# Kernel tuning notes

Measured on AMD Instinct MI355X. Metric: run time of the kernel, lower is better.

Reference implementation:

```python
import jax, jax.numpy as jnp
import numpy as np

INIT_STDEV = 0.01

def setup_inputs() -> dict:
    key = jax.random.key(0)
    k1, k2, k3 = jax.random.split(key, 3)
    B, S, D = 8, 4096, 768
    x = jax.random.normal(k1, (B, S, D), dtype=jnp.float32)
    att_v = jax.random.normal(k2, (D,), dtype=jnp.float32) * INIT_STDEV
    att_W = jax.random.normal(k3, (D, D), dtype=jnp.float32) * INIT_STDEV
    return {"x": x, "att_v": att_v, "att_W": att_W}

def reference(x, att_v, att_W):
    # y = x @ W : [B,S,D]; scores = tanh(y) . v over D : [B,S]
    y = jnp.tanh(jnp.einsum('bsd,de->bse', x, att_W))
    scores = jnp.einsum('bsd,d->bs', y, att_v)
    weights = jax.nn.softmax(scores, axis=-1)            # softmax over sequence
    out = jnp.einsum('bs,bsd->bd', weights, x)           # attsum pool
    return out.astype(jnp.float32)
```

## Files before the change

kernel.cpp:

```cpp
#include <hip/hip_runtime.h>
#include <hip/hip_bf16.h>

constexpr int Bb = 8;
constexpr int Ss = 4096;
constexpr int Dd = 768;
constexpr int Mm = Bb * Ss;

typedef __bf16 bf16x8 __attribute__((ext_vector_type(8)));
typedef float f32x4 __attribute__((ext_vector_type(4)));

__device__ __forceinline__ float fast_tanh(float x) {
    return 1.f - 2.f / (__expf(2.f * x) + 1.f);
}

__device__ __forceinline__ void load_lds16(const void* g, void* l) {
    __builtin_amdgcn_global_load_lds(
        (const __attribute__((address_space(1))) unsigned int*)g,
        (__attribute__((address_space(3))) unsigned int*)l, 16, 0, 0);
}

__global__ __launch_bounds__(256) void convW(const float* __restrict__ W,
                                             __bf16* __restrict__ Wt) {
    __shared__ float tile[32][33];
    const int tx = threadIdx.x & 31;
    const int ty = threadIdx.x >> 5;
    const int kb = blockIdx.x * 32;
    const int nb = blockIdx.y * 32;
#pragma unroll
    for (int i = 0; i < 32; i += 8)
        tile[ty + i][tx] = W[(size_t)(kb + ty + i) * Dd + nb + tx];
    __syncthreads();
#pragma unroll
    for (int i = 0; i < 32; i += 8) {
        const int n = nb + ty + i;
        const int txs = (tx & 7) | ((((tx >> 3) & 3) ^ ((n >> 1) & 3)) << 3);
        Wt[(size_t)n * Dd + kb + txs] = (__bf16)tile[tx][ty + i];
    }
}

__global__ __launch_bounds__(512, 4) void scores_gemm(
    const float* __restrict__ x, const __bf16* __restrict__ Wt,
    const float* __restrict__ v, float* __restrict__ scores3) {
    __shared__ float  As[2][4096];
    __shared__ __bf16 Bs[3][256 * 32];

    const int t = threadIdx.x;
    const int id = blockIdx.x;
    const int ids = ((id & 7) * 96) + (id >> 3);
    const int mb = ids / 3;
    const int nb = ids - mb * 3;
    const int lane = t & 63;
    const int wave = t >> 6;
    const int wm = wave >> 2;
    const int wn = wave & 3;
    const int quad = lane >> 4;
    const int lid = lane & 15;
    const int rslot = ((quad ^ ((lid >> 1) & 3)) * 8);

    const int sarow = t >> 2;
    const float* axg0 = x + (size_t)(mb * 128 + sarow) * Dd + (t & 3) * 4;
    const float* axg1 = x + (size_t)(mb * 128 + sarow) * Dd + 16 + (((t & 3) ^ 1) * 4);

    const __bf16* bgp[2];
    int blp[2];
#pragma unroll
    for (int j = 0; j < 2; ++j) {
        const int flat = j * 8192 + t * 16;
        const int col = flat >> 6;
        bgp[j] = Wt + (size_t)(nb * 256 + col) * Dd + ((flat & 63) >> 1);
        blp[j] = flat >> 1;
    }

    const int p_ = quad >> 1;
    const int sA0 = ((quad & 1) * 2 + 0) ^ p_;
    const int sA1 = ((quad & 1) * 2 + 1) ^ p_;
    const int abase = p_ * 2048 + sA0 * 4;
    const int abase1 = p_ * 2048 + sA1 * 4;

    f32x4 acc[4][4];
#pragma unroll
    for (int tm = 0; tm < 4; ++tm)
#pragma unroll
        for (int nt = 0; nt < 4; ++nt) acc[tm][nt] = (f32x4){0.f, 0.f, 0.f, 0.f};

    load_lds16(axg0, &As[0][t * 4]);
    load_lds16(axg1, &As[0][2048 + t * 4]);
#pragma unroll
    for (int j = 0; j < 2; ++j) load_lds16(bgp[j], &Bs[0][blp[j]]);
#pragma unroll
    for (int j = 0; j < 2; ++j) load_lds16(bgp[j] + 32, &Bs[1][blp[j]]);

#pragma unroll
    for (int k = 0; k < 24; ++k) {
        if (k == 23) asm volatile("s_waitcnt vmcnt(0)" ::: "memory");
        else         asm volatile("s_waitcnt vmcnt(2)" ::: "memory");
        __builtin_amdgcn_sched_barrier(0);
        __builtin_amdgcn_s_barrier();
        __builtin_amdgcn_sched_barrier(0);

        if (k < 23) {
            load_lds16(axg0 + (k + 1) * 32, &As[(k + 1) & 1][t * 4]);
            load_lds16(axg1 + (k + 1) * 32, &As[(k + 1) & 1][2048 + t * 4]);
        }
        if (k < 22) {
#pragma unroll
            for (int j = 0; j < 2; ++j)
                load_lds16(bgp[j] + (k + 2) * 32, &Bs[(k + 2) % 3][blp[j]]);
        }
        __builtin_amdgcn_sched_barrier(0);

        bf16x8 af[4], bfr[4];
#pragma unroll
        for (int tm = 0; tm < 4; ++tm) {
            const int row = wm * 64 + tm * 16 + lid;
            const f32x4 r1 = *(const f32x4*)(&As[k & 1][abase + row * 16]);
            const f32x4 r2 = *(const f32x4*)(&As[k & 1][abase1 + row * 16]);
            bf16x8 a;
            a[0] = (__bf16)r1[0]; a[1] = (__bf16)r1[1];
            a[2] = (__bf16)r1[2]; a[3] = (__bf16)r1[3];
            a[4] = (__bf16)r2[0]; a[5] = (__bf16)r2[1];
            a[6] = (__bf16)r2[2]; a[7] = (__bf16)r2[3];
            af[tm] = a;
        }
#pragma unroll
        for (int nt = 0; nt < 4; ++nt)
            bfr[nt] = *(const bf16x8*)(&Bs[k % 3][(wn * 64 + nt * 16 + lid) * 32 + rslot]);

        __builtin_amdgcn_s_setprio(1);
#pragma unroll
        for (int tm = 0; tm < 4; ++tm)
#pragma unroll
            for (int nt = 0; nt < 4; ++nt)
                acc[tm][nt] = __builtin_amdgcn_mfma_f32_16x16x32_bf16(af[tm], bfr[nt], acc[tm][nt], 0, 0, 0);
        __builtin_amdgcn_s_setprio(0);
    }

    __syncthreads();
    float* ssc = (float*)&Bs[0][0];

    float vv[4];
#pragma unroll
    for (int nt = 0; nt < 4; ++nt)
        vv[nt] = v[nb * 256 + wn * 64 + nt * 16 + lid];

#pragma unroll
    for (int tm = 0; tm < 4; ++tm)
#pragma unroll
        for (int r = 0; r < 4; ++r) {
            float s = 0.f;
#pragma unroll
            for (int nt = 0; nt < 4; ++nt) s += vv[nt] * fast_tanh(acc[tm][nt][r]);
            s += __shfl_xor(s, 1);
            s += __shfl_xor(s, 2);
            s += __shfl_xor(s, 4);
            s += __shfl_xor(s, 8);
            if (lid == 0) ssc[wave * 64 + tm * 16 + quad * 4 + r] = s;
        }
    __syncthreads();
    if (t < 128) {
        const int wmh = t >> 6;
        const int rl = t & 63;
        float s = 0.f;
#pragma unroll
        for (int ww = 0; ww < 4; ++ww) s += ssc[(wmh * 4 + ww) * 64 + rl];
        scores3[(size_t)nb * Mm + mb * 128 + t] = s;
    }
}

__global__ __launch_bounds__(256) void softmax_k(const float* __restrict__ scores3,
                                                 float* __restrict__ weights,
                                                 float* __restrict__ sinv) {
    const int b = blockIdx.x;
    const int t = threadIdx.x;
    const float* s0 = scores3 + (size_t)b * Ss;
    const float* s1 = s0 + Mm;
    const float* s2 = s1 + Mm;
    float* wgt = weights + (size_t)b * Ss;
    __shared__ float red[256];

    float mx = -1e30f;
    for (int i = t; i < Ss; i += 256) {
        const float sc = s0[i] + s1[i] + s2[i];
        wgt[i] = sc;
        mx = fmaxf(mx, sc);
    }
    red[t] = mx;
    __syncthreads();
    for (int o = 128; o > 0; o >>= 1) {
        if (t < o) red[t] = fmaxf(red[t], red[t + o]);
        __syncthreads();
    }
    mx = red[0];
    __syncthreads();
    float sum = 0.f;
    for (int i = t; i < Ss; i += 256) {
        const float e = __expf(wgt[i] - mx);
        wgt[i] = e;
        sum += e;
    }
    red[t] = sum;
    __syncthreads();
    for (int o = 128; o > 0; o >>= 1) {
        if (t < o) red[t] += red[t + o];
        __syncthreads();
    }
    if (t == 0) sinv[b] = 1.f / red[0];
}

__global__ __launch_bounds__(192) void pool1(const float* __restrict__ x,
                                             const float* __restrict__ weights,
                                             float* __restrict__ partial) {
    const int b = blockIdx.y;
    const int c = blockIdx.x;
    const int t = threadIdx.x;
    const float* base = x + ((size_t)b * Ss + c * 32) * Dd;
    const float* wrow = weights + (size_t)b * Ss + c * 32;
    float4 acc = make_float4(0.f, 0.f, 0.f, 0.f);
#pragma unroll 8
    for (int i = 0; i < 32; ++i) {
        const float ww = wrow[i];
        const float4 xv = *(const float4*)(base + (size_t)i * Dd + t * 4);
        acc.x += ww * xv.x;
        acc.y += ww * xv.y;
        acc.z += ww * xv.z;
        acc.w += ww * xv.w;
    }
    *(float4*)(partial + ((size_t)(b * 128 + c)) * Dd + t * 4) = acc;
}

__global__ __launch_bounds__(128) void pool2(const float* __restrict__ partial,
                                             const float* __restrict__ sinv,
                                             float* __restrict__ out) {
    const int b = blockIdx.y;
    const int d = blockIdx.x * 128 + threadIdx.x;
    float s = 0.f;
#pragma unroll 8
    for (int c = 0; c < 128; ++c) s += partial[((size_t)(b * 128 + c)) * Dd + d];
    out[(size_t)b * Dd + d] = s * sinv[b];
}

extern "C" void kernel_launch(void* const* d_in, const int* in_sizes, int n_in,
                              void* d_out, int out_size, void* d_ws, size_t ws_size,
                              hipStream_t stream) {
    (void)in_sizes; (void)n_in; (void)ws_size; (void)out_size;
    const float* x = (const float*)d_in[0];
    const float* v = (const float*)d_in[1];
    const float* W = (const float*)d_in[2];

    char* ws = (char*)d_ws;
    constexpr size_t OFF_WT = 0;
    constexpr size_t OFF_SC = 1179648;
    constexpr size_t OFF_WG = OFF_SC + 393216;
    constexpr size_t OFF_SI = OFF_WG + 131072;
    constexpr size_t OFF_PA = OFF_SI + 128;

    __bf16* Wt     = (__bf16*)(ws + OFF_WT);
    float* scores3 = (float*)(ws + OFF_SC);
    float* weights = (float*)(ws + OFF_WG);
    float* sinv    = (float*)(ws + OFF_SI);
    float* partial = (float*)(ws + OFF_PA);

    convW<<<dim3(Dd / 32, Dd / 32), 256, 0, stream>>>(W, Wt);
    scores_gemm<<<dim3(3 * Mm / 128), 512, 0, stream>>>(x, Wt, v, scores3);
    softmax_k<<<dim3(Bb), 256, 0, stream>>>(scores3, weights, sinv);
    pool1<<<dim3(128, Bb), 192, 0, stream>>>(x, weights, partial);
    pool2<<<dim3(6, Bb), 128, 0, stream>>>(partial, sinv, (float*)d_out);
}
```

Before: 242.6 us.

## Pre-convert x to bf16 and fuse softmax and final reduction into pooling

```diff
diff --git a/kernel.cpp b/kernel.cpp
--- a/kernel.cpp
+++ b/kernel.cpp
@@ -19,32 +19,49 @@
         (__attribute__((address_space(3))) unsigned int*)l, 16, 0, 0);
 }
 
-__global__ __launch_bounds__(256) void convW(const float* __restrict__ W,
-                                             __bf16* __restrict__ Wt) {
-    __shared__ float tile[32][33];
-    const int tx = threadIdx.x & 31;
-    const int ty = threadIdx.x >> 5;
-    const int kb = blockIdx.x * 32;
-    const int nb = blockIdx.y * 32;
-#pragma unroll
-    for (int i = 0; i < 32; i += 8)
-        tile[ty + i][tx] = W[(size_t)(kb + ty + i) * Dd + nb + tx];
-    __syncthreads();
-#pragma unroll
-    for (int i = 0; i < 32; i += 8) {
-        const int n = nb + ty + i;
-        const int txs = (tx & 7) | ((((tx >> 3) & 3) ^ ((n >> 1) & 3)) << 3);
-        Wt[(size_t)n * Dd + kb + txs] = (__bf16)tile[tx][ty + i];
+__global__ __launch_bounds__(256) void convWX(const float* __restrict__ W,
+                                              __bf16* __restrict__ Wt,
+                                              const float* __restrict__ x,
+                                              __bf16* __restrict__ xb) {
+    const int bid = blockIdx.x;
+    if (bid < 576) {
+        __shared__ float tile[32][33];
+        const int tx = threadIdx.x & 31;
+        const int ty = threadIdx.x >> 5;
+        const int kb = (bid % 24) * 32;
+        const int nb = (bid / 24) * 32;
+#pragma unroll
+        for (int i = 0; i < 32; i += 8)
+            tile[ty + i][tx] = W[(size_t)(kb + ty + i) * Dd + nb + tx];
+        __syncthreads();
+#pragma unroll
+        for (int i = 0; i < 32; i += 8) {
+            const int n = nb + ty + i;
+            const int txs = (tx & 7) | ((((tx >> 3) & 3) ^ ((n >> 1) & 3)) << 3);
+            Wt[(size_t)n * Dd + kb + txs] = (__bf16)tile[tx][ty + i];
+        }
+    } else {
+        const size_t i = ((size_t)(bid - 576) * 256 + threadIdx.x) * 8;
+        const float4 a = *(const float4*)(x + i);
+        const float4 b = *(const float4*)(x + i + 4);
+        bf16x8 p;
+        p[0] = (__bf16)a.x; p[1] = (__bf16)a.y; p[2] = (__bf16)a.z; p[3] = (__bf16)a.w;
+        p[4] = (__bf16)b.x; p[5] = (__bf16)b.y; p[6] = (__bf16)b.z; p[7] = (__bf16)b.w;
+        *(bf16x8*)(xb + i) = p;
     }
 }
 
 __global__ __launch_bounds__(512, 4) void scores_gemm(
-    const float* __restrict__ x, const __bf16* __restrict__ Wt,
-    const float* __restrict__ v, float* __restrict__ scores3) {
-    __shared__ float  As[2][4096];
+    const __bf16* __restrict__ xb, const __bf16* __restrict__ Wt,
+    const float* __restrict__ v, float* __restrict__ scores3,
+    unsigned int* __restrict__ counter) {
+    __shared__ __bf16 As[3][128 * 32];
     __shared__ __bf16 Bs[3][256 * 32];
+    __shared__ float ssc[8][64];
 
     const int t = threadIdx.x;
+    if (blockIdx.x == 0 && t < 8) counter[t] = 0u;
+
     const int id = blockIdx.x;
     const int ids = ((id & 7) * 96) + (id >> 3);
     const int mb = ids / 3;
@@ -57,9 +74,8 @@
     const int lid = lane & 15;
     const int rslot = ((quad ^ ((lid >> 1) & 3)) * 8);
 
-    const int sarow = t >> 2;
-    const float* axg0 = x + (size_t)(mb * 128 + sarow) * Dd + (t & 3) * 4;
-    const float* axg1 = x + (size_t)(mb * 128 + sarow) * Dd + 16 + (((t & 3) ^ 1) * 4);
+    const __bf16* axg = xb + (size_t)(mb * 128 + (t >> 2)) * Dd + (t & 3) * 8;
+    const int awl = t * 8;
 
     const __bf16* bgp[2];
     int blp[2];
@@ -71,38 +87,29 @@
         blp[j] = flat >> 1;
     }
 
-    const int p_ = quad >> 1;
-    const int sA0 = ((quad & 1) * 2 + 0) ^ p_;
-    const int sA1 = ((quad & 1) * 2 + 1) ^ p_;
-    const int abase = p_ * 2048 + sA0 * 4;
-    const int abase1 = p_ * 2048 + sA1 * 4;
-
     f32x4 acc[4][4];
 #pragma unroll
     for (int tm = 0; tm < 4; ++tm)
 #pragma unroll
         for (int nt = 0; nt < 4; ++nt) acc[tm][nt] = (f32x4){0.f, 0.f, 0.f, 0.f};
 
-    load_lds16(axg0, &As[0][t * 4]);
-    load_lds16(axg1, &As[0][2048 + t * 4]);
+    load_lds16(axg, &As[0][awl]);
 #pragma unroll
     for (int j = 0; j < 2; ++j) load_lds16(bgp[j], &Bs[0][blp[j]]);
+    load_lds16(axg + 32, &As[1][awl]);
 #pragma unroll
     for (int j = 0; j < 2; ++j) load_lds16(bgp[j] + 32, &Bs[1][blp[j]]);
 
 #pragma unroll
     for (int k = 0; k < 24; ++k) {
         if (k == 23) asm volatile("s_waitcnt vmcnt(0)" ::: "memory");
-        else         asm volatile("s_waitcnt vmcnt(2)" ::: "memory");
+        else         asm volatile("s_waitcnt vmcnt(3)" ::: "memory");
         __builtin_amdgcn_sched_barrier(0);
         __builtin_amdgcn_s_barrier();
         __builtin_amdgcn_sched_barrier(0);
 
-        if (k < 23) {
-            load_lds16(axg0 + (k + 1) * 32, &As[(k + 1) & 1][t * 4]);
-            load_lds16(axg1 + (k + 1) * 32, &As[(k + 1) & 1][2048 + t * 4]);
-        }
         if (k < 22) {
+            load_lds16(axg + (k + 2) * 32, &As[(k + 2) % 3][awl]);
 #pragma unroll
             for (int j = 0; j < 2; ++j)
                 load_lds16(bgp[j] + (k + 2) * 32, &Bs[(k + 2) % 3][blp[j]]);
@@ -111,17 +118,8 @@
 
         bf16x8 af[4], bfr[4];
 #pragma unroll
-        for (int tm = 0; tm < 4; ++tm) {
-            const int row = wm * 64 + tm * 16 + lid;
-            const f32x4 r1 = *(const f32x4*)(&As[k & 1][abase + row * 16]);
-            const f32x4 r2 = *(const f32x4*)(&As[k & 1][abase1 + row * 16]);
-            bf16x8 a;
-            a[0] = (__bf16)r1[0]; a[1] = (__bf16)r1[1];
-            a[2] = (__bf16)r1[2]; a[3] = (__bf16)r1[3];
-            a[4] = (__bf16)r2[0]; a[5] = (__bf16)r2[1];
-            a[6] = (__bf16)r2[2]; a[7] = (__bf16)r2[3];
-            af[tm] = a;
-        }
+        for (int tm = 0; tm < 4; ++tm)
+            af[tm] = *(const bf16x8*)(&As[k % 3][(wm * 64 + tm * 16 + lid) * 32 + quad * 8]);
 #pragma unroll
         for (int nt = 0; nt < 4; ++nt)
             bfr[nt] = *(const bf16x8*)(&Bs[k % 3][(wn * 64 + nt * 16 + lid) * 32 + rslot]);
@@ -134,9 +132,6 @@
                 acc[tm][nt] = __builtin_amdgcn_mfma_f32_16x16x32_bf16(af[tm], bfr[nt], acc[tm][nt], 0, 0, 0);
         __builtin_amdgcn_s_setprio(0);
     }
-
-    __syncthreads();
-    float* ssc = (float*)&Bs[0][0];
 
     float vv[4];
 #pragma unroll
@@ -154,7 +149,7 @@
             s += __shfl_xor(s, 2);
             s += __shfl_xor(s, 4);
             s += __shfl_xor(s, 8);
-            if (lid == 0) ssc[wave * 64 + tm * 16 + quad * 4 + r] = s;
+            if (lid == 0) ssc[wave][tm * 16 + quad * 4 + r] = s;
         }
     __syncthreads();
     if (t < 128) {
@@ -162,63 +157,34 @@
         const int rl = t & 63;
         float s = 0.f;
 #pragma unroll
-        for (int ww = 0; ww < 4; ++ww) s += ssc[(wmh * 4 + ww) * 64 + rl];
+        for (int ww = 0; ww < 4; ++ww) s += ssc[wmh * 4 + ww][rl];
         scores3[(size_t)nb * Mm + mb * 128 + t] = s;
     }
 }
 
-__global__ __launch_bounds__(256) void softmax_k(const float* __restrict__ scores3,
-                                                 float* __restrict__ weights,
-                                                 float* __restrict__ sinv) {
-    const int b = blockIdx.x;
-    const int t = threadIdx.x;
-    const float* s0 = scores3 + (size_t)b * Ss;
-    const float* s1 = s0 + Mm;
-    const float* s2 = s1 + Mm;
-    float* wgt = weights + (size_t)b * Ss;
-    __shared__ float red[256];
-
-    float mx = -1e30f;
-    for (int i = t; i < Ss; i += 256) {
-        const float sc = s0[i] + s1[i] + s2[i];
-        wgt[i] = sc;
-        mx = fmaxf(mx, sc);
-    }
-    red[t] = mx;
-    __syncthreads();
-    for (int o = 128; o > 0; o >>= 1) {
-        if (t < o) red[t] = fmaxf(red[t], red[t + o]);
-        __syncthreads();
-    }
-    mx = red[0];
-    __syncthreads();
-    float sum = 0.f;
-    for (int i = t; i < Ss; i += 256) {
-        const float e = __expf(wgt[i] - mx);
-        wgt[i] = e;
-        sum += e;
-    }
-    red[t] = sum;
-    __syncthreads();
-    for (int o = 128; o > 0; o >>= 1) {
-        if (t < o) red[t] += red[t + o];
-        __syncthreads();
-    }
-    if (t == 0) sinv[b] = 1.f / red[0];
-}
-
-__global__ __launch_bounds__(192) void pool1(const float* __restrict__ x,
-                                             const float* __restrict__ weights,
-                                             float* __restrict__ partial) {
+__global__ __launch_bounds__(192) void pool_all(const float* __restrict__ x,
+                                                const float* __restrict__ scores3,
+                                                float* __restrict__ partial,
+                                                float* __restrict__ esum,
+                                                unsigned int* __restrict__ counter,
+                                                float* __restrict__ out) {
     const int b = blockIdx.y;
     const int c = blockIdx.x;
     const int t = threadIdx.x;
+    __shared__ float we[32];
+    __shared__ int isLast;
+
+    if (t < 32) {
+        const size_t i = (size_t)b * Ss + c * 32 + t;
+        we[t] = __expf(scores3[i] + scores3[Mm + i] + scores3[2 * Mm + i]);
+    }
+    __syncthreads();
+
     const float* base = x + ((size_t)b * Ss + c * 32) * Dd;
-    const float* wrow = weights + (size_t)b * Ss + c * 32;
     float4 acc = make_float4(0.f, 0.f, 0.f, 0.f);
 #pragma unroll 8
     for (int i = 0; i < 32; ++i) {
-        const float ww = wrow[i];
+        const float ww = we[i];
         const float4 xv = *(const float4*)(base + (size_t)i * Dd + t * 4);
         acc.x += ww * xv.x;
         acc.y += ww * xv.y;
@@ -226,17 +192,48 @@
         acc.w += ww * xv.w;
     }
     *(float4*)(partial + ((size_t)(b * 128 + c)) * Dd + t * 4) = acc;
-}
-
-__global__ __launch_bounds__(128) void pool2(const float* __restrict__ partial,
-                                             const float* __restrict__ sinv,
-                                             float* __restrict__ out) {
-    const int b = blockIdx.y;
-    const int d = blockIdx.x * 128 + threadIdx.x;
-    float s = 0.f;
+    if (t == 0) {
+        float s = 0.f;
+#pragma unroll
+        for (int i = 0; i < 32; ++i) s += we[i];
+        esum[b * 128 + c] = s;
+    }
+
+    __syncthreads();
+    if (t == 0) {
+        __threadfence();
+        isLast = (atomicAdd(&counter[b], 1u) == 127u);
+    }
+    __syncthreads();
+    if (!isLast) return;
+    __threadfence();
+
+    float es = 0.f;
+    if (t < 64) {
+        es = esum[b * 128 + t] + esum[b * 128 + 64 + t];
+        es += __shfl_xor(es, 1);
+        es += __shfl_xor(es, 2);
+        es += __shfl_xor(es, 4);
+        es += __shfl_xor(es, 8);
+        es += __shfl_xor(es, 16);
+        es += __shfl_xor(es, 32);
+    }
+    __shared__ float esT;
+    if (t == 0) esT = es;
+    __syncthreads();
+    const float inv = 1.f / esT;
+
+    float4 s4 = make_float4(0.f, 0.f, 0.f, 0.f);
 #pragma unroll 8
-    for (int c = 0; c < 128; ++c) s += partial[((size_t)(b * 128 + c)) * Dd + d];
-    out[(size_t)b * Dd + d] = s * sinv[b];
+    for (int cc = 0; cc < 128; ++cc) {
+        const float4 p = *(const float4*)(partial + ((size_t)(b * 128 + cc)) * Dd + t * 4);
+        s4.x += p.x; s4.y += p.y; s4.z += p.z; s4.w += p.w;
+    }
+    float* o = out + (size_t)b * Dd + t * 4;
+    o[0] = s4.x * inv;
+    o[1] = s4.y * inv;
+    o[2] = s4.z * inv;
+    o[3] = s4.w * inv;
 }
 
 extern "C" void kernel_launch(void* const* d_in, const int* in_sizes, int n_in,
@@ -248,21 +245,22 @@
     const float* W = (const float*)d_in[2];
 
     char* ws = (char*)d_ws;
-    constexpr size_t OFF_WT = 0;
-    constexpr size_t OFF_SC = 1179648;
-    constexpr size_t OFF_WG = OFF_SC + 393216;
-    constexpr size_t OFF_SI = OFF_WG + 131072;
-    constexpr size_t OFF_PA = OFF_SI + 128;
-
-    __bf16* Wt     = (__bf16*)(ws + OFF_WT);
-    float* scores3 = (float*)(ws + OFF_SC);
-    float* weights = (float*)(ws + OFF_WG);
-    float* sinv    = (float*)(ws + OFF_SI);
-    float* partial = (float*)(ws + OFF_PA);
-
-    convW<<<dim3(Dd / 32, Dd / 32), 256, 0, stream>>>(W, Wt);
-    scores_gemm<<<dim3(3 * Mm / 128), 512, 0, stream>>>(x, Wt, v, scores3);
-    softmax_k<<<dim3(Bb), 256, 0, stream>>>(scores3, weights, sinv);
-    pool1<<<dim3(128, Bb), 192, 0, stream>>>(x, weights, partial);
-    pool2<<<dim3(6, Bb), 128, 0, stream>>>(partial, sinv, (float*)d_out);
-}
+    constexpr size_t OFF_WT  = 0;
+    constexpr size_t OFF_SC  = 1179648;
+    constexpr size_t OFF_CNT = OFF_SC + 393216;
+    constexpr size_t OFF_ES  = OFF_CNT + 128;
+    constexpr size_t OFF_PA  = OFF_ES + 4096;
+    constexpr size_t OFF_XB  = OFF_PA + 3145728;
+
+    __bf16* Wt            = (__bf16*)(ws + OFF_WT);
+    float* scores3        = (float*)(ws + OFF_SC);
+    unsigned int* counter = (unsigned int*)(ws + OFF_CNT);
+    float* esum           = (float*)(ws + OFF_ES);
+    float* partial        = (float*)(ws + OFF_PA);
+    __bf16* xb            = (__bf16*)(ws + OFF_XB);
+
+    convWX<<<dim3(576 + (Mm * Dd) / (256 * 8)), 256, 0, stream>>>(W, Wt, x, xb);
+    scores_gemm<<<dim3(3 * Mm / 128), 512, 0, stream>>>(xb, Wt, v, scores3, counter);
+    pool_all<<<dim3(128, Bb), 192, 0, stream>>>(x, scores3, partial, esum, counter,
+                                                (float*)d_out);
+}
```

New measurement: 264.6 us. +9.1%, slower.
